# Kernel optimization log

Measured on AMD Instinct MI355X. Metric: run time of the kernel, lower is better.

Reference implementation:

```python
import jax, jax.numpy as jnp
import numpy as np
import math

H = 16          # n_heads
D = 1024        # hidden_dim
HD = D // H     # head_dim = 64
LR = 256        # Linformer low-rank length L
MAX_T = 4096    # max_seq_len


def setup_inputs() -> dict:
    key = jax.random.key(0)
    ks = jax.random.split(key, 7)
    X = jax.random.normal(ks[0], (4, 4096, D), dtype=jnp.float32)
    # lecun_normal ~ N(0, 1/fan_in)
    W_kernel = jax.random.normal(ks[1], (D, 3 * D), dtype=jnp.float32) / math.sqrt(D)
    W_bias = jnp.zeros((3 * D,), dtype=jnp.float32)
    low_rank_E = jax.random.normal(ks[2], (MAX_T, H, LR), dtype=jnp.float32) / math.sqrt(MAX_T)
    low_rank_V = jax.random.normal(ks[3], (MAX_T, H, LR), dtype=jnp.float32) / math.sqrt(MAX_T)
    o_kernel = jax.random.normal(ks[4], (D, D), dtype=jnp.float32) / math.sqrt(D)
    o_bias = jnp.zeros((D,), dtype=jnp.float32)
    return {"X": X, "W_kernel": W_kernel, "W_bias": W_bias,
            "low_rank_E": low_rank_E, "low_rank_V": low_rank_V,
            "o_kernel": o_kernel, "o_bias": o_bias}


def reference(X, W_kernel, W_bias, low_rank_E, low_rank_V, o_kernel, o_bias):
    B, T, _ = X.shape
    # L2-normalize tokens
    norm = jnp.linalg.norm(X, ord=2, axis=-1, keepdims=True)  # (B,T,1)
    Xn = X / norm
    # fused QKV projection
    qkv = Xn @ W_kernel + W_bias                 # (B,T,3D)
    qkv = qkv.reshape(B, T, 3, H, HD)
    Q, K, V = qkv[:, :, 0], qkv[:, :, 1], qkv[:, :, 2]   # (B,T,H,HD)
    # low-rank sequence projection of K/V: T -> L
    E = low_rank_E[:T]                            # (T,H,L)
    F = low_rank_V[:T]                            # (T,H,L)
    Kp = jnp.einsum('THK,BTHD->BHKD', E, K)       # (B,H,L,HD)
    Vp = jnp.einsum('THK,BTHD->BHKD', F, V)       # (B,H,L,HD)
    Qh = Q.transpose(0, 2, 1, 3)                  # (B,H,T,HD)
    logits = jnp.einsum('BHTD,BHKD->BHTK', Qh, Kp) / math.sqrt(HD)
    attn = jax.nn.softmax(logits, axis=-1)        # (B,H,T,L)
    out = jnp.einsum('BHTK,BHKD->BHTD', attn, Vp) # (B,H,T,HD)
    out = out.transpose(0, 2, 1, 3).reshape(B, T, H * HD)
    return out @ o_kernel + o_bias
```

## Files before the change

kernel.cpp:

```cpp
#include <hip/hip_runtime.h>
#include <stdint.h>

typedef unsigned short u16;
typedef uint32_t u32;
typedef __bf16 bf16x8 __attribute__((ext_vector_type(8)));
typedef float f32x4 __attribute__((ext_vector_type(4)));

__device__ __forceinline__ u16 f2bf(float f) {
    u32 u = __builtin_bit_cast(u32, f);
    u += 0x7fffu + ((u >> 16) & 1u);
    return (u16)(u >> 16);
}

__device__ __forceinline__ f32x4 mfma16(bf16x8 a, bf16x8 b, f32x4 c) {
    return __builtin_amdgcn_mfma_f32_16x16x32_bf16(a, b, c, 0, 0, 0);
}

__device__ __forceinline__ void gld_lds16(void* lds, const void* g) {
    __builtin_amdgcn_global_load_lds(
        (__attribute__((address_space(1))) void*)(uintptr_t)g,
        (__attribute__((address_space(3))) void*)(u32)(uintptr_t)lds,
        16, 0, 0);
}

__global__ __launch_bounds__(256) void k_norm(const float* __restrict__ X,
                                              u16* __restrict__ Xn) {
    const int row = blockIdx.x;
    const float4 v = ((const float4*)(X + (size_t)row * 1024))[threadIdx.x];
    float ss = v.x * v.x + v.y * v.y + v.z * v.z + v.w * v.w;
#pragma unroll
    for (int m = 1; m < 64; m <<= 1) ss += __shfl_xor(ss, m);
    __shared__ float red[4];
    if ((threadIdx.x & 63) == 0) red[threadIdx.x >> 6] = ss;
    __syncthreads();
    const float sc = 1.0f / sqrtf(red[0] + red[1] + red[2] + red[3]);
    ushort4 o;
    o.x = f2bf(v.x * sc); o.y = f2bf(v.y * sc);
    o.z = f2bf(v.z * sc); o.w = f2bf(v.w * sc);
    ((ushort4*)(Xn + (size_t)row * 1024))[threadIdx.x] = o;
}

__global__ __launch_bounds__(256) void k_transpose_cast64(
    const float* __restrict__ src, u16* __restrict__ dst,
    int R, int rstride, long zsrc, long zdst) {
    __shared__ float tile[64][65];
    src += (size_t)blockIdx.z * zsrc;
    dst += (size_t)blockIdx.z * zdst;
    const int c0 = blockIdx.x * 64, r0 = blockIdx.y * 64;
    const int tid = threadIdx.x;
    const int lr = tid >> 4, lc = tid & 15;
#pragma unroll
    for (int i = 0; i < 4; ++i) {
        const int r = lr + i * 16;
        const float4 v = *(const float4*)(src + (size_t)(r0 + r) * rstride + c0 + lc * 4);
        tile[r][lc * 4 + 0] = v.x; tile[r][lc * 4 + 1] = v.y;
        tile[r][lc * 4 + 2] = v.z; tile[r][lc * 4 + 3] = v.w;
    }
    __syncthreads();
    const int c = tid >> 2, seg = tid & 3;
    u32 w[8];
#pragma unroll
    for (int j = 0; j < 8; ++j) {
        const u32 lo = f2bf(tile[seg * 16 + 2 * j][c]);
        const u32 hi = f2bf(tile[seg * 16 + 2 * j + 1][c]);
        w[j] = lo | (hi << 16);
    }
    u16* dp = dst + (size_t)(c0 + c) * R + r0 + seg * 16;
    uint4 q0; q0.x = w[0]; q0.y = w[1]; q0.z = w[2]; q0.w = w[3];
    uint4 q1; q1.x = w[4]; q1.y = w[5]; q1.z = w[6]; q1.w = w[7];
    *(uint4*)dp = q0;
    *((uint4*)dp + 1) = q1;
}

#define G8_PRE(Aptr, Bptr)                                                       \
    const int tid = threadIdx.x, lane = tid & 63;                                \
    const int wid = tid >> 6, wm = wid >> 2, wn = wid & 3;                       \
    const int cl = lane & 15, g = lane >> 4;                                     \
    const int colb = (tid & 7) * 16;                                             \
    const int scb = colb ^ (((tid >> 3) & 7) << 4);                              \
    const int rbA = ((tid >> 3) & 31) + ((tid >> 8) << 7);                       \
    const int rbB = tid >> 3;                                                    \
    const char* gA = (const char*)(Aptr) + (size_t)(m0 + rbA) * 2048 + scb;      \
    const char* gB = (const char*)(Bptr) + (size_t)(n0 + rbB) * 2048 + scb;      \
    const u32 lA = (u32)(rbA * 128 + colb);                                      \
    const u32 lB = (u32)(65536 + rbB * 128 + colb);                              \
    const int xr0 = (g * 16) ^ ((cl & 7) << 4);                                  \
    const int xr1 = (64 + g * 16) ^ ((cl & 7) << 4);

#define G8_STA(q, tau, beta) gld_lds16(sm + (beta) + lA + (q) * 4096,            \
                                       gA + (q) * 65536 + (size_t)(tau) * 128);
#define G8_STB(c, tau, beta) gld_lds16(sm + (beta) + lB + (c) * 8192,            \
                                       gB + (c) * 131072 + (size_t)(tau) * 128);

#define G8_RDB(beta)                                                             \
    _Pragma("unroll") for (int nf = 0; nf < 4; ++nf) {                           \
        const u32 rb_ = (beta) + 65536 + (u32)(wn * 64 + nf * 16 + cl) * 128;    \
        bF[nf][0] = *(const bf16x8*)(sm + rb_ + xr0);                            \
        bF[nf][1] = *(const bf16x8*)(sm + rb_ + xr1);                            \
    }
#define G8_RDA2(dst, q, beta)                                                    \
    _Pragma("unroll") for (int m = 0; m < 2; ++m) {                              \
        const u32 ra_ = (beta) + (u32)(wm * 128 + (q) * 32 + m * 16 + cl) * 128; \
        dst[m][0] = *(const bf16x8*)(sm + ra_ + xr0);                            \
        dst[m][1] = *(const bf16x8*)(sm + ra_ + xr1);                            \
    }

#define G8_WAIT4 asm volatile("s_waitcnt lgkmcnt(4)" ::: "memory");              \
    __builtin_amdgcn_sched_barrier(0);
#define G8_WAIT0 asm volatile("s_waitcnt lgkmcnt(0)" ::: "memory");              \
    __builtin_amdgcn_sched_barrier(0);

#define G8_MMA(q, SRC)                                                           \
    __builtin_amdgcn_s_setprio(1);                                               \
    _Pragma("unroll") for (int m = 0; m < 2; ++m)                                \
        _Pragma("unroll") for (int nf = 0; nf < 4; ++nf) {                       \
            acc[(q)*2 + m][nf] = mfma16(SRC[m][0], bF[nf][0], acc[(q)*2 + m][nf]);\
            acc[(q)*2 + m][nf] = mfma16(SRC[m][1], bF[nf][1], acc[(q)*2 + m][nf]);\
        }                                                                        \
    __builtin_amdgcn_s_setprio(0);                                               \
    __builtin_amdgcn_s_barrier();                                                \
    __builtin_amdgcn_sched_barrier(0);

#define G8_LOOP                                                                  \
    bf16x8 aFe[2][2], aFo[2][2], bF[4][2];                                       \
    G8_STA(0, 0, 0) G8_STB(0, 0, 0) G8_STA(1, 0, 0) G8_STB(1, 0, 0)              \
    G8_STA(2, 0, 0) G8_STB(2, 0, 0) G8_STA(3, 0, 0) G8_STB(3, 0, 0)              \
    G8_STA(0, 1, 32768) G8_STB(0, 1, 32768)                                      \
    G8_STA(1, 1, 32768) G8_STB(1, 1, 32768)                                      \
    G8_STA(2, 1, 32768) G8_STB(2, 1, 32768)                                      \
    for (int it = 0; it < 8; ++it) {                                             \
        const int t1 = 2 * it + 1, t2v = 2 * it + 2, t3v = 2 * it + 3;           \
        const bool nt = (it < 7);                                                \
                                                                         \
        G8_STA(3, t1, 32768) G8_STB(3, t1, 32768)                                \
        asm volatile("s_waitcnt vmcnt(8)" ::: "memory");                         \
        __builtin_amdgcn_s_barrier();                                            \
        G8_RDB(0) G8_RDA2(aFe, 0, 0) G8_RDA2(aFo, 1, 0)                          \
        G8_WAIT4 G8_MMA(0, aFe)                                                  \
                                                                         \
        if (nt) { G8_STA(0, t2v, 0) G8_STB(0, t2v, 0) }                          \
        G8_RDA2(aFe, 2, 0)                                                       \
        G8_WAIT4 G8_MMA(1, aFo)                                                  \
                                                                         \
        if (nt) { G8_STA(1, t2v, 0) G8_STB(1, t2v, 0) }                          \
        G8_RDA2(aFo, 3, 0)                                                       \
        G8_WAIT4 G8_MMA(2, aFe)                                                  \
                                                                         \
        if (nt) { G8_STA(2, t2v, 0) G8_STB(2, t2v, 0) }                          \
        G8_WAIT0 G8_MMA(3, aFo)                                                  \
                                                                         \
        if (nt) {                                                                \
            G8_STA(3, t2v, 0) G8_STB(3, t2v, 0)                                  \
            asm volatile("s_waitcnt vmcnt(8)" ::: "memory");                     \
        } else {                                                                 \
            asm volatile("s_waitcnt vmcnt(0)" ::: "memory");                     \
        }                                                                        \
        __builtin_amdgcn_s_barrier();                                            \
        G8_RDB(32768) G8_RDA2(aFe, 0, 32768) G8_RDA2(aFo, 1, 32768)              \
        G8_WAIT4 G8_MMA(0, aFe)                                                  \
                                                                         \
        if (nt) { G8_STA(0, t3v, 32768) G8_STB(0, t3v, 32768) }                  \
        G8_RDA2(aFe, 2, 32768)                                                   \
        G8_WAIT4 G8_MMA(1, aFo)                                                  \
                                                                         \
        if (nt) { G8_STA(1, t3v, 32768) G8_STB(1, t3v, 32768) }                  \
        G8_RDA2(aFo, 3, 32768)                                                   \
        G8_WAIT4 G8_MMA(2, aFe)                                                  \
                                                                         \
        if (nt) { G8_STA(2, t3v, 32768) G8_STB(2, t3v, 32768) }                  \
        G8_WAIT0 G8_MMA(3, aFo)                                                  \
    }

__global__ __launch_bounds__(512, 2) void k_gemm_qkv(
    const u16* __restrict__ A, const u16* __restrict__ Bt,
    const float* __restrict__ bias,
    u16* __restrict__ Qo, u16* __restrict__ Kt, u16* __restrict__ Vt) {
    __shared__ __align__(16) char sm[131072];
    u32 bid = blockIdx.x;
    bid = (bid & 7) * 96 + (bid >> 3);
    const int m0 = (int)(bid / 12) * 256, n0 = (int)(bid % 12) * 256;

    G8_PRE(A, Bt)

    const f32x4 fz = {0.f, 0.f, 0.f, 0.f};
    f32x4 acc[8][4];
#pragma unroll
    for (int i = 0; i < 8; ++i)
#pragma unroll
        for (int j = 0; j < 4; ++j) acc[i][j] = fz;

    G8_LOOP

#pragma unroll
    for (int mf = 0; mf < 8; ++mf) {
        const int mbase = m0 + wm * 128 + mf * 16 + g * 4;
        const int b = mbase >> 12;
        const int t = mbase & 4095;
#pragma unroll
        for (int nf = 0; nf < 4; ++nf) {
            const int n = n0 + wn * 64 + nf * 16 + cl;
            const float bv = bias[n];
            const int seg = n >> 10;
            const int hd = n & 1023;
            f32x4 v = acc[mf][nf];
            if (seg == 0) {
#pragma unroll
                for (int r = 0; r < 4; ++r)
                    Qo[(size_t)(mbase + r) * 1024 + hd] = f2bf(v[r] + bv);
            } else {
                u16* dst = (seg == 1) ? Kt : Vt;
                ushort4 pk;
                pk.x = f2bf(v[0] + bv); pk.y = f2bf(v[1] + bv);
                pk.z = f2bf(v[2] + bv); pk.w = f2bf(v[3] + bv);
                *(ushort4*)(dst + (size_t)(b * 1024 + hd) * 4096 + t) = pk;
            }
        }
    }
}

__global__ __launch_bounds__(512, 2) void k_gemm_out(
    const u16* __restrict__ A, const u16* __restrict__ Bt,
    const float* __restrict__ bias, float* __restrict__ out) {
    __shared__ __align__(16) char sm[131072];
    u32 bid = blockIdx.x;
    bid = (bid & 7) * 32 + (bid >> 3);
    const int m0 = (int)(bid / 4) * 256, n0 = (int)(bid % 4) * 256;

    G8_PRE(A, Bt)

    const f32x4 fz = {0.f, 0.f, 0.f, 0.f};
    f32x4 acc[8][4];
#pragma unroll
    for (int i = 0; i < 8; ++i)
#pragma unroll
        for (int j = 0; j < 4; ++j) acc[i][j] = fz;

    G8_LOOP

#pragma unroll
    for (int mf = 0; mf < 8; ++mf) {
        const int mbase = m0 + wm * 128 + mf * 16 + g * 4;
#pragma unroll
        for (int nf = 0; nf < 4; ++nf) {
            const int n = n0 + wn * 64 + nf * 16 + cl;
            const float bv = bias[n];
            f32x4 v = acc[mf][nf];
#pragma unroll
            for (int r = 0; r < 4; ++r)
                out[(size_t)(mbase + r) * 1024 + n] = v[r] + bv;
        }
    }
}

__global__ __launch_bounds__(512) void k_gemm_kpvp(
    const u16* __restrict__ Et, const u16* __restrict__ Ft,
    const u16* __restrict__ Kt, const u16* __restrict__ Vt,
    float* __restrict__ Pp) {
    __shared__ __align__(16) char sm[49152];
    const int tid = threadIdx.x, lane = tid & 63, wid = tid >> 6;
    const int wm = wid >> 2, wn = wid & 3;
    const int cl = lane & 15, g = lane >> 4;
    const int mT = blockIdx.x;
    const int hs = blockIdx.y;
    const int h = hs & 15, s = hs >> 4;
    const int ks = blockIdx.z;

    const int rA = tid >> 2, c16 = tid & 3;
    const int scol = (c16 ^ ((rA >> 1) & 3)) * 8;
    const u16 *gA, *gB0, *gB1;
    if (s == 0) {
        gA = Et + (size_t)h * (256 * 4096) + (size_t)(mT * 128 + rA) * 4096
             + ks * 1024 + scol;
        gB0 = Kt + (size_t)((((rA >> 6) * 16 + h) * 64) + (rA & 63)) * 4096
              + ks * 1024 + scol;
        const int rB1 = rA + 128;
        gB1 = Kt + (size_t)((((rB1 >> 6) * 16 + h) * 64) + (rB1 & 63)) * 4096
              + ks * 1024 + scol;
    } else {
        const int dc = mT * 128 + rA;
        gA = Vt + (size_t)(((dc >> 6) * 16 + h) * 64 + (dc & 63)) * 4096
             + ks * 1024 + scol;
        gB0 = Ft + (size_t)h * (256 * 4096) + (size_t)rA * 4096 + ks * 1024 + scol;
        gB1 = gB0 + (size_t)128 * 4096;
    }
    const u32 lA = (u32)(rA * 64 + c16 * 16);
    const u32 lB0 = (u32)(8192 + rA * 64 + c16 * 16);
    const u32 lB1 = lB0 + 128 * 64;
    const int xsw = (g ^ ((cl >> 1) & 3)) * 16;

    const f32x4 fz = {0.f, 0.f, 0.f, 0.f};
    f32x4 acc[4][4];
#pragma unroll
    for (int i = 0; i < 4; ++i)
#pragma unroll
        for (int j = 0; j < 4; ++j) acc[i][j] = fz;

    gld_lds16(sm + lA, gA); gld_lds16(sm + lB0, gB0); gld_lds16(sm + lB1, gB1);

    u32 roff = 0;
    for (int kt = 0; kt < 32; ++kt) {
        const u32 woff = roff ^ 24576;
        if (kt < 31) {
            gld_lds16(sm + woff + lA, gA + (kt + 1) * 32);
            gld_lds16(sm + woff + lB0, gB0 + (kt + 1) * 32);
            gld_lds16(sm + woff + lB1, gB1 + (kt + 1) * 32);
            asm volatile("s_waitcnt vmcnt(3)" ::: "memory");
        } else {
            asm volatile("s_waitcnt vmcnt(0)" ::: "memory");
        }
        __builtin_amdgcn_s_barrier();
        __builtin_amdgcn_sched_barrier(0);
        const char* rb = sm + roff;
        bf16x8 aF[4], bF[4];
#pragma unroll
        for (int mf = 0; mf < 4; ++mf)
            aF[mf] = *(const bf16x8*)(rb + (wm * 64 + mf * 16 + cl) * 64 + xsw);
#pragma unroll
        for (int nf = 0; nf < 4; ++nf)
            bF[nf] = *(const bf16x8*)(rb + 8192 + (wn * 64 + nf * 16 + cl) * 64 + xsw);
        asm volatile("s_waitcnt lgkmcnt(0)" ::: "memory");
        __builtin_amdgcn_sched_barrier(0);
        __builtin_amdgcn_s_setprio(1);
#pragma unroll
        for (int mf = 0; mf < 4; ++mf)
#pragma unroll
            for (int nf = 0; nf < 4; ++nf)
                acc[mf][nf] = mfma16(aF[mf], bF[nf], acc[mf][nf]);
        __builtin_amdgcn_s_setprio(0);
        asm volatile("s_waitcnt lgkmcnt(0)" ::: "memory");
        __builtin_amdgcn_s_barrier();
        roff = woff;
    }

    float* P = Pp + ((size_t)(ks * 32 + hs) << 16);
#pragma unroll
    for (int mf = 0; mf < 4; ++mf) {
        const int m = mT * 128 + wm * 64 + mf * 16 + g * 4;
#pragma unroll
        for (int nf = 0; nf < 4; ++nf) {
            const int nn = wn * 64 + nf * 16 + cl;
            f32x4 v = acc[mf][nf];
#pragma unroll
            for (int r = 0; r < 4; ++r)
                P[(size_t)(m + r) * 256 + nn] = v[r];
        }
    }
}

__global__ __launch_bounds__(256) void k_red(const float* __restrict__ Pp,
                                             u16* __restrict__ Kp,
                                             u16* __restrict__ Vpt) {
    const int e = blockIdx.x * 256 + threadIdx.x;
    const int hs = e >> 14;
    const int rem = (e & 16383) * 4;
    float4 sum = {0.f, 0.f, 0.f, 0.f};
#pragma unroll
    for (int ks = 0; ks < 4; ++ks) {
        const float4 v = *(const float4*)(Pp + (((size_t)(ks * 32 + hs)) << 16) + rem);
        sum.x += v.x; sum.y += v.y; sum.z += v.z; sum.w += v.w;
    }
    const int m = rem >> 8, col = rem & 255;
    const int h = hs & 15, sf = hs >> 4;
    ushort4 pk;
    pk.x = f2bf(sum.x); pk.y = f2bf(sum.y);
    pk.z = f2bf(sum.z); pk.w = f2bf(sum.w);
    if (sf == 0) {
        const int bh = (col >> 6) * 16 + h, d0 = col & 63;
        *(ushort4*)(Kp + (size_t)bh * 16384 + m * 64 + d0) = pk;
    } else {
        const int bh = (m >> 6) * 16 + h, d = m & 63;
        *(ushort4*)(Vpt + (size_t)bh * 16384 + d * 256 + col) = pk;
    }
}

__global__ __launch_bounds__(256, 1) void k_attn(
    const u16* __restrict__ Q, const u16* __restrict__ Kp,
    const u16* __restrict__ Vpt, u16* __restrict__ AO) {
    __shared__ __align__(16) char sm[65536];
    const int lane = threadIdx.x & 63, wid = threadIdx.x >> 6;
    const int cl = lane & 15, g = lane >> 4;
    const int tT = blockIdx.x, h = blockIdx.y, b = blockIdx.z;
    const int bh = b * 16 + h;
    const int trow0 = b * 4096 + tT * 128 + wid * 32;
    const u16* Qb = Q + (size_t)trow0 * 1024 + h * 64;
    const u16* KpB = Kp + (size_t)bh * (256 * 64);
    const u16* VpB = Vpt + (size_t)bh * (64 * 256);
    char* sP = sm + wid * 16384;

    bf16x8 qF[2][2];
#pragma unroll
    for (int nf = 0; nf < 2; ++nf)
#pragma unroll
        for (int ks = 0; ks < 2; ++ks)
            qF[nf][ks] = *(const bf16x8*)(Qb + (size_t)(nf * 16 + cl) * 1024 + ks * 32 + g * 8);

    const f32x4 fz = {0.f, 0.f, 0.f, 0.f};
    f32x4 Sp[16][2];
#pragma unroll
    for (int mf = 0; mf < 16; ++mf) { Sp[mf][0] = fz; Sp[mf][1] = fz; }

#pragma unroll
    for (int mf = 0; mf < 16; ++mf) {
#pragma unroll
        for (int ks = 0; ks < 2; ++ks) {
            bf16x8 aF = *(const bf16x8*)(KpB + (size_t)(mf * 16 + cl) * 64 + ks * 32 + g * 8);
            Sp[mf][0] = mfma16(aF, qF[0][ks], Sp[mf][0]);
            Sp[mf][1] = mfma16(aF, qF[1][ks], Sp[mf][1]);
        }
    }

    float inv_sum[2];
#pragma unroll
    for (int nf = 0; nf < 2; ++nf) {
        float mx = -1e30f;
#pragma unroll
        for (int mf = 0; mf < 16; ++mf)
#pragma unroll
            for (int r = 0; r < 4; ++r) {
                float x = Sp[mf][nf][r] * 0.125f;
                Sp[mf][nf][r] = x;
                mx = fmaxf(mx, x);
            }
        mx = fmaxf(mx, __shfl_xor(mx, 16));
        mx = fmaxf(mx, __shfl_xor(mx, 32));
        float sum = 0.f;
#pragma unroll
        for (int mf = 0; mf < 16; ++mf)
#pragma unroll
            for (int r = 0; r < 4; ++r) {
                float p = __expf(Sp[mf][nf][r] - mx);
                Sp[mf][nf][r] = p;
                sum += p;
            }
        sum += __shfl_xor(sum, 16);
        sum += __shfl_xor(sum, 32);
        inv_sum[nf] = 1.0f / sum;

        const int tl = nf * 16 + cl;
        const int sw = (tl & 7) << 4;
#pragma unroll
        for (int mf = 0; mf < 16; ++mf) {
            uint2 pk;
            pk.x = (u32)f2bf(Sp[mf][nf][0]) | ((u32)f2bf(Sp[mf][nf][1]) << 16);
            pk.y = (u32)f2bf(Sp[mf][nf][2]) | ((u32)f2bf(Sp[mf][nf][3]) << 16);
            *(uint2*)(sP + ((tl * 512 + (mf * 16 + g * 4) * 2) ^ sw)) = pk;
        }
    }

    f32x4 Oa[4][2];
#pragma unroll
    for (int mf = 0; mf < 4; ++mf) { Oa[mf][0] = fz; Oa[mf][1] = fz; }
#pragma unroll
    for (int ks = 0; ks < 8; ++ks) {
        bf16x8 aF[4];
#pragma unroll
        for (int mf = 0; mf < 4; ++mf)
            aF[mf] = *(const bf16x8*)(VpB + (size_t)(mf * 16 + cl) * 256 + ks * 32 + g * 8);
#pragma unroll
        for (int nf = 0; nf < 2; ++nf) {
            const int tl = nf * 16 + cl;
            const int sw = (tl & 7) << 4;
            bf16x8 bF = *(const bf16x8*)(sP + ((tl * 512 + (ks * 32 + g * 8) * 2) ^ sw));
#pragma unroll
            for (int mf = 0; mf < 4; ++mf)
                Oa[mf][nf] = mfma16(aF[mf], bF, Oa[mf][nf]);
        }
    }

#pragma unroll
    for (int nf = 0; nf < 2; ++nf) {
        const int t = trow0 + nf * 16 + cl;
#pragma unroll
        for (int mf = 0; mf < 4; ++mf) {
            f32x4 v = Oa[mf][nf];
            ushort4 pk;
            pk.x = f2bf(v[0] * inv_sum[nf]); pk.y = f2bf(v[1] * inv_sum[nf]);
            pk.z = f2bf(v[2] * inv_sum[nf]); pk.w = f2bf(v[3] * inv_sum[nf]);
            *(ushort4*)(AO + (size_t)t * 1024 + h * 64 + mf * 16 + g * 4) = pk;
        }
    }
}

extern "C" void kernel_launch(void* const* d_in, const int* in_sizes, int n_in,
                              void* d_out, int out_size, void* d_ws, size_t ws_size,
                              hipStream_t stream) {
    const float* X  = (const float*)d_in[0];
    const float* Wk = (const float*)d_in[1];
    const float* Wb = (const float*)d_in[2];
    const float* E  = (const float*)d_in[3];
    const float* F  = (const float*)d_in[4];
    const float* Ok = (const float*)d_in[5];
    const float* Ob = (const float*)d_in[6];
    float* out = (float*)d_out;
    char* ws = (char*)d_ws;

    u16* Xn  = (u16*)(ws + 0);
    u16* Wt  = (u16*)(ws + 33554432);
    u16* Ot  = (u16*)(ws + 39845888);
    u16* Et  = (u16*)(ws + 41943040);
    u16* Ft  = (u16*)(ws + 75497472);
    u16* Qb  = (u16*)(ws + 109051904);
    u16* Kt  = (u16*)(ws + 142606336);
    u16* Vt  = (u16*)(ws + 176160768);
    u16* Kp  = (u16*)(ws + 209715200);
    u16* Vpt = (u16*)(ws + 211812352);
    float* Pp = (float*)(ws + 0);
    u16* AO  = Xn;

    k_norm<<<16384, 256, 0, stream>>>(X, Xn);
    k_transpose_cast64<<<dim3(48, 16, 1), 256, 0, stream>>>(Wk, Wt, 1024, 3072, 0, 0);
    k_transpose_cast64<<<dim3(16, 16, 1), 256, 0, stream>>>(Ok, Ot, 1024, 1024, 0, 0);
    k_transpose_cast64<<<dim3(4, 64, 16), 256, 0, stream>>>(E, Et, 4096, 4096, 256, 1048576);
    k_transpose_cast64<<<dim3(4, 64, 16), 256, 0, stream>>>(F, Ft, 4096, 4096, 256, 1048576);
    k_gemm_qkv<<<768, 512, 0, stream>>>(Xn, Wt, Wb, Qb, Kt, Vt);
    k_gemm_kpvp<<<dim3(2, 32, 4), 512, 0, stream>>>(Et, Ft, Kt, Vt, Pp);
    k_red<<<2048, 256, 0, stream>>>(Pp, Kp, Vpt);
    k_attn<<<dim3(32, 16, 4), 256, 0, stream>>>(Qb, Kp, Vpt, AO);
    k_gemm_out<<<256, 512, 0, stream>>>(AO, Ot, Ob, out);
}
```

Measured before the change: 365.6 us.

## Drop split-K partials in Kp/Vp GEMM and write bf16 outputs directly

The low-rank K/V projection GEMM no longer splits the 4096-long sequence reduction into four partial sums written as fp32 and then summed by a separate reduction kernel. Each block now covers the full reduction for one batch, head and 128-row tile, with smaller 2x2 MFMA accumulators per wave and a wider 64-element K step. Results are packed to bf16 and stored straight into the Kp and Vpt layouts. This removes the fp32 partial buffer traffic and one kernel launch, at the cost of longer per-block loops, and the grid size (256 blocks) stays the same.

```diff
diff --git a/kernel.cpp b/kernel.cpp
--- a/kernel.cpp
+++ b/kernel.cpp
@@ -255,55 +255,46 @@
 __global__ __launch_bounds__(512) void k_gemm_kpvp(
     const u16* __restrict__ Et, const u16* __restrict__ Ft,
     const u16* __restrict__ Kt, const u16* __restrict__ Vt,
-    float* __restrict__ Pp) {
+    u16* __restrict__ Kp, u16* __restrict__ Vpt) {
     __shared__ __align__(16) char sm[49152];
     const int tid = threadIdx.x, lane = tid & 63, wid = tid >> 6;
-    const int wm = wid >> 2, wn = wid & 3;
     const int cl = lane & 15, g = lane >> 4;
-    const int mT = blockIdx.x;
-    const int hs = blockIdx.y;
+    const int xT = blockIdx.x;
+    const int b  = blockIdx.y;
+    const int hs = blockIdx.z;
     const int h = hs & 15, s = hs >> 4;
-    const int ks = blockIdx.z;
-
-    const int rA = tid >> 2, c16 = tid & 3;
-    const int scol = (c16 ^ ((rA >> 1) & 3)) * 8;
-    const u16 *gA, *gB0, *gB1;
-    if (s == 0) {
-        gA = Et + (size_t)h * (256 * 4096) + (size_t)(mT * 128 + rA) * 4096
-             + ks * 1024 + scol;
-        gB0 = Kt + (size_t)((((rA >> 6) * 16 + h) * 64) + (rA & 63)) * 4096
-              + ks * 1024 + scol;
-        const int rB1 = rA + 128;
-        gB1 = Kt + (size_t)((((rB1 >> 6) * 16 + h) * 64) + (rB1 & 63)) * 4096
-              + ks * 1024 + scol;
-    } else {
-        const int dc = mT * 128 + rA;
-        gA = Vt + (size_t)(((dc >> 6) * 16 + h) * 64 + (dc & 63)) * 4096
-             + ks * 1024 + scol;
-        gB0 = Ft + (size_t)h * (256 * 4096) + (size_t)rA * 4096 + ks * 1024 + scol;
-        gB1 = gB0 + (size_t)128 * 4096;
-    }
-    const u32 lA = (u32)(rA * 64 + c16 * 16);
-    const u32 lB0 = (u32)(8192 + rA * 64 + c16 * 16);
-    const u32 lB1 = lB0 + 128 * 64;
-    const int xsw = (g ^ ((cl >> 1) & 3)) * 16;
+    const int bh = b * 16 + h;
+
+    const int rp = tid >> 3, c16 = tid & 7;
+    const u16* P = (s ? Ft : Et) + (size_t)h * (256 * 4096);
+    const u16* S = (s ? Vt : Kt) + (size_t)bh * (64 * 4096);
+    const char* gP0 = (const char*)(P + (size_t)(xT * 128 + rp) * 4096)
+                      + ((c16 ^ (rp & 7)) * 16);
+    const char* gP1 = (const char*)(P + (size_t)(xT * 128 + rp + 64) * 4096)
+                      + ((c16 ^ ((rp + 64) & 7)) * 16);
+    const char* gS0 = (const char*)(S + (size_t)rp * 4096)
+                      + ((c16 ^ (rp & 7)) * 16);
+    const u32 lP0 = (u32)(rp * 128 + c16 * 16);
+    const u32 lP1 = (u32)((rp + 64) * 128 + c16 * 16);
+    const u32 lS0 = (u32)(16384 + rp * 128 + c16 * 16);
+
+    int wa, wb; u32 baseA, baseB;
+    if (s == 0) { wa = wid >> 1; wb = wid & 1; baseA = 0;     baseB = 16384; }
+    else        { wa = wid >> 2; wb = wid & 3; baseA = 16384; baseB = 0;     }
 
     const f32x4 fz = {0.f, 0.f, 0.f, 0.f};
-    f32x4 acc[4][4];
-#pragma unroll
-    for (int i = 0; i < 4; ++i)
-#pragma unroll
-        for (int j = 0; j < 4; ++j) acc[i][j] = fz;
-
-    gld_lds16(sm + lA, gA); gld_lds16(sm + lB0, gB0); gld_lds16(sm + lB1, gB1);
+    f32x4 acc[2][2];
+    acc[0][0] = fz; acc[0][1] = fz; acc[1][0] = fz; acc[1][1] = fz;
+
+    gld_lds16(sm + lP0, gP0); gld_lds16(sm + lP1, gP1); gld_lds16(sm + lS0, gS0);
 
     u32 roff = 0;
-    for (int kt = 0; kt < 32; ++kt) {
+    for (int kt = 0; kt < 64; ++kt) {
         const u32 woff = roff ^ 24576;
-        if (kt < 31) {
-            gld_lds16(sm + woff + lA, gA + (kt + 1) * 32);
-            gld_lds16(sm + woff + lB0, gB0 + (kt + 1) * 32);
-            gld_lds16(sm + woff + lB1, gB1 + (kt + 1) * 32);
+        if (kt < 63) {
+            gld_lds16(sm + woff + lP0, gP0 + (kt + 1) * 128);
+            gld_lds16(sm + woff + lP1, gP1 + (kt + 1) * 128);
+            gld_lds16(sm + woff + lS0, gS0 + (kt + 1) * 128);
             asm volatile("s_waitcnt vmcnt(3)" ::: "memory");
         } else {
             asm volatile("s_waitcnt vmcnt(0)" ::: "memory");
@@ -311,65 +302,66 @@
         __builtin_amdgcn_s_barrier();
         __builtin_amdgcn_sched_barrier(0);
         const char* rb = sm + roff;
-        bf16x8 aF[4], bF[4];
-#pragma unroll
-        for (int mf = 0; mf < 4; ++mf)
-            aF[mf] = *(const bf16x8*)(rb + (wm * 64 + mf * 16 + cl) * 64 + xsw);
-#pragma unroll
-        for (int nf = 0; nf < 4; ++nf)
-            bF[nf] = *(const bf16x8*)(rb + 8192 + (wn * 64 + nf * 16 + cl) * 64 + xsw);
+        bf16x8 aF[2][2], bFr[2][2];
+#pragma unroll
+        for (int mf = 0; mf < 2; ++mf) {
+            const int row = wa * 32 + mf * 16 + cl;
+            const u32 base = baseA + (u32)row * 128;
+            const int sw = (row & 7) << 4;
+            aF[mf][0] = *(const bf16x8*)(rb + base + ((g * 16) ^ sw));
+            aF[mf][1] = *(const bf16x8*)(rb + base + ((64 + g * 16) ^ sw));
+        }
+#pragma unroll
+        for (int nf = 0; nf < 2; ++nf) {
+            const int row = wb * 32 + nf * 16 + cl;
+            const u32 base = baseB + (u32)row * 128;
+            const int sw = (row & 7) << 4;
+            bFr[nf][0] = *(const bf16x8*)(rb + base + ((g * 16) ^ sw));
+            bFr[nf][1] = *(const bf16x8*)(rb + base + ((64 + g * 16) ^ sw));
+        }
         asm volatile("s_waitcnt lgkmcnt(0)" ::: "memory");
         __builtin_amdgcn_sched_barrier(0);
         __builtin_amdgcn_s_setprio(1);
 #pragma unroll
-        for (int mf = 0; mf < 4; ++mf)
-#pragma unroll
-            for (int nf = 0; nf < 4; ++nf)
-                acc[mf][nf] = mfma16(aF[mf], bF[nf], acc[mf][nf]);
+        for (int mf = 0; mf < 2; ++mf)
+#pragma unroll
+            for (int nf = 0; nf < 2; ++nf) {
+                acc[mf][nf] = mfma16(aF[mf][0], bFr[nf][0], acc[mf][nf]);
+                acc[mf][nf] = mfma16(aF[mf][1], bFr[nf][1], acc[mf][nf]);
+            }
         __builtin_amdgcn_s_setprio(0);
-        asm volatile("s_waitcnt lgkmcnt(0)" ::: "memory");
         __builtin_amdgcn_s_barrier();
         roff = woff;
     }
 
-    float* P = Pp + ((size_t)(ks * 32 + hs) << 16);
-#pragma unroll
-    for (int mf = 0; mf < 4; ++mf) {
-        const int m = mT * 128 + wm * 64 + mf * 16 + g * 4;
-#pragma unroll
-        for (int nf = 0; nf < 4; ++nf) {
-            const int nn = wn * 64 + nf * 16 + cl;
-            f32x4 v = acc[mf][nf];
-#pragma unroll
-            for (int r = 0; r < 4; ++r)
-                P[(size_t)(m + r) * 256 + nn] = v[r];
-        }
-    }
-}
-
-__global__ __launch_bounds__(256) void k_red(const float* __restrict__ Pp,
-                                             u16* __restrict__ Kp,
-                                             u16* __restrict__ Vpt) {
-    const int e = blockIdx.x * 256 + threadIdx.x;
-    const int hs = e >> 14;
-    const int rem = (e & 16383) * 4;
-    float4 sum = {0.f, 0.f, 0.f, 0.f};
-#pragma unroll
-    for (int ks = 0; ks < 4; ++ks) {
-        const float4 v = *(const float4*)(Pp + (((size_t)(ks * 32 + hs)) << 16) + rem);
-        sum.x += v.x; sum.y += v.y; sum.z += v.z; sum.w += v.w;
-    }
-    const int m = rem >> 8, col = rem & 255;
-    const int h = hs & 15, sf = hs >> 4;
-    ushort4 pk;
-    pk.x = f2bf(sum.x); pk.y = f2bf(sum.y);
-    pk.z = f2bf(sum.z); pk.w = f2bf(sum.w);
-    if (sf == 0) {
-        const int bh = (col >> 6) * 16 + h, d0 = col & 63;
-        *(ushort4*)(Kp + (size_t)bh * 16384 + m * 64 + d0) = pk;
+    if (s == 0) {
+        u16* O = Kp + (size_t)bh * 16384;
+#pragma unroll
+        for (int mf = 0; mf < 2; ++mf) {
+            const int kl = xT * 128 + wa * 32 + mf * 16 + g * 4;
+#pragma unroll
+            for (int nf = 0; nf < 2; ++nf) {
+                const int d = wb * 32 + nf * 16 + cl;
+                f32x4 v = acc[mf][nf];
+#pragma unroll
+                for (int r = 0; r < 4; ++r)
+                    O[(size_t)(kl + r) * 64 + d] = f2bf(v[r]);
+            }
+        }
     } else {
-        const int bh = (m >> 6) * 16 + h, d = m & 63;
-        *(ushort4*)(Vpt + (size_t)bh * 16384 + d * 256 + col) = pk;
+        u16* O = Vpt + (size_t)bh * 16384;
+#pragma unroll
+        for (int mf = 0; mf < 2; ++mf) {
+            const int d = wa * 32 + mf * 16 + g * 4;
+#pragma unroll
+            for (int nf = 0; nf < 2; ++nf) {
+                const int kl = xT * 128 + wb * 32 + nf * 16 + cl;
+                f32x4 v = acc[mf][nf];
+#pragma unroll
+                for (int r = 0; r < 4; ++r)
+                    O[(size_t)(d + r) * 256 + kl] = f2bf(v[r]);
+            }
+        }
     }
 }
 
@@ -504,7 +496,6 @@
     u16* Vt  = (u16*)(ws + 176160768);
     u16* Kp  = (u16*)(ws + 209715200);
     u16* Vpt = (u16*)(ws + 211812352);
-    float* Pp = (float*)(ws + 0);
     u16* AO  = Xn;
 
     k_norm<<<16384, 256, 0, stream>>>(X, Xn);
@@ -513,8 +504,7 @@
     k_transpose_cast64<<<dim3(4, 64, 16), 256, 0, stream>>>(E, Et, 4096, 4096, 256, 1048576);
     k_transpose_cast64<<<dim3(4, 64, 16), 256, 0, stream>>>(F, Ft, 4096, 4096, 256, 1048576);
     k_gemm_qkv<<<768, 512, 0, stream>>>(Xn, Wt, Wb, Qb, Kt, Vt);
-    k_gemm_kpvp<<<dim3(2, 32, 4), 512, 0, stream>>>(Et, Ft, Kt, Vt, Pp);
-    k_red<<<2048, 256, 0, stream>>>(Pp, Kp, Vpt);
+    k_gemm_kpvp<<<dim3(2, 4, 32), 512, 0, stream>>>(Et, Ft, Kt, Vt, Kp, Vpt);
     k_attn<<<dim3(32, 16, 4), 256, 0, stream>>>(Qb, Kp, Vpt, AO);
     k_gemm_out<<<256, 512, 0, stream>>>(AO, Ot, Ob, out);
 }
```

Result: slower. 374.1 us (+2.3%).

## Merge prep kernels into one launch and stage K/V transpose stores through LDS

Applied to the files above, without the earlier changes.

Replaces the norm kernel and four transpose-cast launches with a single k_prep kernel that dispatches on block index, removing launch gaps and tail idle time between small kernels. In the QKV GEMM epilogue, K/V tiles are now written to shared memory with a rotated layout and then stored to the transposed K/V buffers as contiguous 16-byte rows, instead of scattered 8-byte strided stores. This adds a shared-memory pass and a barrier in the epilogue and makes k_prep blocks heterogeneous.

```diff
diff --git a/kernel.cpp b/kernel.cpp
--- a/kernel.cpp
+++ b/kernel.cpp
@@ -23,35 +23,57 @@
         16, 0, 0);
 }
 
-__global__ __launch_bounds__(256) void k_norm(const float* __restrict__ X,
-                                              u16* __restrict__ Xn) {
-    const int row = blockIdx.x;
-    const float4 v = ((const float4*)(X + (size_t)row * 1024))[threadIdx.x];
-    float ss = v.x * v.x + v.y * v.y + v.z * v.z + v.w * v.w;
-#pragma unroll
-    for (int m = 1; m < 64; m <<= 1) ss += __shfl_xor(ss, m);
-    __shared__ float red[4];
-    if ((threadIdx.x & 63) == 0) red[threadIdx.x >> 6] = ss;
-    __syncthreads();
-    const float sc = 1.0f / sqrtf(red[0] + red[1] + red[2] + red[3]);
-    ushort4 o;
-    o.x = f2bf(v.x * sc); o.y = f2bf(v.y * sc);
-    o.z = f2bf(v.z * sc); o.w = f2bf(v.w * sc);
-    ((ushort4*)(Xn + (size_t)row * 1024))[threadIdx.x] = o;
-}
-
-__global__ __launch_bounds__(256) void k_transpose_cast64(
-    const float* __restrict__ src, u16* __restrict__ dst,
-    int R, int rstride, long zsrc, long zdst) {
+__global__ __launch_bounds__(256) void k_prep(
+    const float* __restrict__ X, u16* __restrict__ Xn,
+    const float* __restrict__ Wk, u16* __restrict__ Wt,
+    const float* __restrict__ Ok, u16* __restrict__ Ot,
+    const float* __restrict__ E, u16* __restrict__ Et,
+    const float* __restrict__ F, u16* __restrict__ Ft) {
     __shared__ float tile[64][65];
-    src += (size_t)blockIdx.z * zsrc;
-    dst += (size_t)blockIdx.z * zdst;
-    const int c0 = blockIdx.x * 64, r0 = blockIdx.y * 64;
     const int tid = threadIdx.x;
+    int bid = blockIdx.x;
+
+    if (bid < 16384) {
+        const int row = bid;
+        const float4 v = ((const float4*)(X + (size_t)row * 1024))[tid];
+        float ss = v.x * v.x + v.y * v.y + v.z * v.z + v.w * v.w;
+#pragma unroll
+        for (int m = 1; m < 64; m <<= 1) ss += __shfl_xor(ss, m);
+        if ((tid & 63) == 0) tile[0][tid >> 6] = ss;
+        __syncthreads();
+        const float sc = 1.0f / sqrtf(tile[0][0] + tile[0][1] + tile[0][2] + tile[0][3]);
+        ushort4 o;
+        o.x = f2bf(v.x * sc); o.y = f2bf(v.y * sc);
+        o.z = f2bf(v.z * sc); o.w = f2bf(v.w * sc);
+        ((ushort4*)(Xn + (size_t)row * 1024))[tid] = o;
+        return;
+    }
+    bid -= 16384;
+    const float* src; u16* dst; int R, rstride, c0, r0;
+    if (bid < 768) {
+        src = Wk; dst = Wt; R = 1024; rstride = 3072;
+        c0 = (bid % 48) * 64; r0 = (bid / 48) * 64;
+    } else if (bid < 1024) {
+        const int t = bid - 768;
+        src = Ok; dst = Ot; R = 1024; rstride = 1024;
+        c0 = (t & 15) * 64; r0 = (t >> 4) * 64;
+    } else if (bid < 5120) {
+        const int t = bid - 1024;
+        const int x = t & 3, y = (t >> 2) & 63, z = t >> 8;
+        src = E + (size_t)z * 256; dst = Et + (size_t)z * 1048576;
+        R = 4096; rstride = 4096;
+        c0 = x * 64; r0 = y * 64;
+    } else {
+        const int t = bid - 5120;
+        const int x = t & 3, y = (t >> 2) & 63, z = t >> 8;
+        src = F + (size_t)z * 256; dst = Ft + (size_t)z * 1048576;
+        R = 4096; rstride = 4096;
+        c0 = x * 64; r0 = y * 64;
+    }
     const int lr = tid >> 4, lc = tid & 15;
 #pragma unroll
     for (int i = 0; i < 4; ++i) {
-        const int r = lr + i * 16;
+        const int r = lr + 16 * i;
         const float4 v = *(const float4*)(src + (size_t)(r0 + r) * rstride + c0 + lc * 4);
         tile[r][lc * 4 + 0] = v.x; tile[r][lc * 4 + 1] = v.y;
         tile[r][lc * 4 + 2] = v.z; tile[r][lc * 4 + 3] = v.w;
@@ -191,29 +213,48 @@
 
     G8_LOOP
 
-#pragma unroll
-    for (int mf = 0; mf < 8; ++mf) {
-        const int mbase = m0 + wm * 128 + mf * 16 + g * 4;
-        const int b = mbase >> 12;
-        const int t = mbase & 4095;
-#pragma unroll
-        for (int nf = 0; nf < 4; ++nf) {
-            const int n = n0 + wn * 64 + nf * 16 + cl;
-            const float bv = bias[n];
-            const int seg = n >> 10;
-            const int hd = n & 1023;
-            f32x4 v = acc[mf][nf];
-            if (seg == 0) {
+    const int segb = n0 >> 10;
+    if (segb == 0) {
+#pragma unroll
+        for (int mf = 0; mf < 8; ++mf) {
+            const int mbase = m0 + wm * 128 + mf * 16 + g * 4;
+#pragma unroll
+            for (int nf = 0; nf < 4; ++nf) {
+                const int n = n0 + wn * 64 + nf * 16 + cl;
+                const float bv = bias[n];
+                f32x4 v = acc[mf][nf];
 #pragma unroll
                 for (int r = 0; r < 4; ++r)
-                    Qo[(size_t)(mbase + r) * 1024 + hd] = f2bf(v[r] + bv);
-            } else {
-                u16* dst = (seg == 1) ? Kt : Vt;
-                ushort4 pk;
-                pk.x = f2bf(v[0] + bv); pk.y = f2bf(v[1] + bv);
-                pk.z = f2bf(v[2] + bv); pk.w = f2bf(v[3] + bv);
-                *(ushort4*)(dst + (size_t)(b * 1024 + hd) * 4096 + t) = pk;
+                    Qo[(size_t)(mbase + r) * 1024 + n] = f2bf(v[r] + bv);
             }
+        }
+    } else {
+        u16* dst = (segb == 1) ? Kt : Vt;
+        const int b = m0 >> 12, tbase = m0 & 4095, hd0 = n0 & 1023;
+#pragma unroll
+        for (int mf = 0; mf < 8; ++mf) {
+            const int m = wm * 128 + mf * 16 + g * 4;
+#pragma unroll
+            for (int nf = 0; nf < 4; ++nf) {
+                const int nl = wn * 64 + nf * 16 + cl;
+                const float bv = bias[n0 + nl];
+                f32x4 v = acc[mf][nf];
+                uint2 pk;
+                pk.x = (u32)f2bf(v[0] + bv) | ((u32)f2bf(v[1] + bv) << 16);
+                pk.y = (u32)f2bf(v[2] + bv) | ((u32)f2bf(v[3] + bv) << 16);
+                *(uint2*)(sm + nl * 512 + ((m * 2 + (nl & 31) * 16) & 511)) = pk;
+            }
+        }
+        __syncthreads();
+        const int nl = tid >> 1, half = tid & 1;
+        const u32 rot = (nl & 31) * 16;
+        char* gdst = (char*)(dst + (size_t)(b * 1024 + hd0 + nl) * 4096 + tbase)
+                     + half * 256;
+#pragma unroll
+        for (int c16 = 0; c16 < 16; ++c16) {
+            const u32 c = (u32)(half * 256 + c16 * 16);
+            uint4 q = *(const uint4*)(sm + nl * 512 + ((c + rot) & 511));
+            *(uint4*)(gdst + c16 * 16) = q;
         }
     }
 }
@@ -507,11 +548,7 @@
     float* Pp = (float*)(ws + 0);
     u16* AO  = Xn;
 
-    k_norm<<<16384, 256, 0, stream>>>(X, Xn);
-    k_transpose_cast64<<<dim3(48, 16, 1), 256, 0, stream>>>(Wk, Wt, 1024, 3072, 0, 0);
-    k_transpose_cast64<<<dim3(16, 16, 1), 256, 0, stream>>>(Ok, Ot, 1024, 1024, 0, 0);
-    k_transpose_cast64<<<dim3(4, 64, 16), 256, 0, stream>>>(E, Et, 4096, 4096, 256, 1048576);
-    k_transpose_cast64<<<dim3(4, 64, 16), 256, 0, stream>>>(F, Ft, 4096, 4096, 256, 1048576);
+    k_prep<<<25600, 256, 0, stream>>>(X, Xn, Wk, Wt, Ok, Ot, E, Et, F, Ft);
     k_gemm_qkv<<<768, 512, 0, stream>>>(Xn, Wt, Wb, Qb, Kt, Vt);
     k_gemm_kpvp<<<dim3(2, 32, 4), 512, 0, stream>>>(Et, Ft, Kt, Vt, Pp);
     k_red<<<2048, 256, 0, stream>>>(Pp, Kp, Vpt);
```

Measured after the change: 360.7 us. No clear change (-1.3%).
